# Performance work log

Measured on AMD Instinct MI355X. Metric: run time of the kernel, lower is better.

Reference implementation:

```python
import jax, jax.numpy as jnp
import numpy as np

N_NODES = 10000
N_EDGES = 160000
F_IN = 50          # PPI num_features
H = 4              # attention heads
C_BODY = 256       # body GAT out channels per head -> concat 1024
C_HEAD = 64        # head GAT out channels per head -> concat 256
T = 121            # PPI num_classes (one task head each)
D_BODY = H * C_BODY   # 1024
D_HEAD = H * C_HEAD   # 256


def setup_inputs() -> dict:
    key = jax.random.key(0)
    ks = jax.random.split(key, 18)
    inv = lambda f: 1.0 / np.sqrt(f)
    x = jax.random.normal(ks[0], (N_NODES, F_IN), dtype=jnp.float32)
    edge_index = jax.random.randint(ks[1], (2, N_EDGES), 0, N_NODES, dtype=jnp.int64)
    # body GATConv(50 -> 256, heads=4)
    W_body = jax.random.normal(ks[2], (F_IN, H, C_BODY), jnp.float32) * inv(F_IN)
    a_src_body = jax.random.normal(ks[3], (H, C_BODY), jnp.float32) * 0.1
    a_dst_body = jax.random.normal(ks[4], (H, C_BODY), jnp.float32) * 0.1
    b_body = jnp.zeros((D_BODY,), jnp.float32)
    # body Linear(50 -> 1024)
    Wfc_body = jax.random.normal(ks[5], (F_IN, D_BODY), jnp.float32) * inv(F_IN)
    bfc_body = jnp.zeros((D_BODY,), jnp.float32)
    # stacked per-task head GATConv(1024 -> 64, heads=4)
    Wh = jax.random.normal(ks[6], (T, D_BODY, H, C_HEAD), jnp.float32) * inv(D_BODY)
    a_src_h = jax.random.normal(ks[7], (T, H, C_HEAD), jnp.float32) * 0.1
    a_dst_h = jax.random.normal(ks[8], (T, H, C_HEAD), jnp.float32) * 0.1
    b_h = jnp.zeros((T, D_HEAD), jnp.float32)
    # stacked per-task Linear(1024 -> 256)
    W1 = jax.random.normal(ks[9], (T, D_BODY, D_HEAD), jnp.float32) * inv(D_BODY)
    b1 = jnp.zeros((T, D_HEAD), jnp.float32)
    # stacked per-task Linear(256 -> 2)
    W2 = jax.random.normal(ks[10], (T, D_HEAD, 2), jnp.float32) * inv(D_HEAD)
    b2 = jnp.zeros((T, 2), jnp.float32)
    return dict(x=x, edge_index=edge_index,
                W_body=W_body, a_src_body=a_src_body, a_dst_body=a_dst_body, b_body=b_body,
                Wfc_body=Wfc_body, bfc_body=bfc_body,
                Wh=Wh, a_src_h=a_src_h, a_dst_h=a_dst_h, b_h=b_h,
                W1=W1, b1=b1, W2=W2, b2=b2)


def gat_conv(x, W, a_src, a_dst, bias, src, dst, num_nodes):
    """PyG GATConv (concat=True, negative_slope=0.2). src/dst include self loops."""
    h = jnp.einsum('nf,fhc->nhc', x, W)                      # [N,H,C]
    al_src = jnp.sum(h * a_src, axis=-1)                     # [N,H]
    al_dst = jnp.sum(h * a_dst, axis=-1)                     # [N,H]
    e = jax.nn.leaky_relu(al_src[src] + al_dst[dst], 0.2)    # [E,H]
    # segment softmax over incoming edges of each target node
    m = jax.lax.stop_gradient(jax.ops.segment_max(e, dst, num_segments=num_nodes))
    ex = jnp.exp(e - m[dst])
    denom = jax.ops.segment_sum(ex, dst, num_segments=num_nodes)
    alpha = ex / (denom[dst] + 1e-16)                        # [E,H]
    out = jax.ops.segment_sum(alpha[:, :, None] * h[src], dst, num_segments=num_nodes)
    return out.reshape(num_nodes, -1) + bias                 # [N,H*C]


def reference(x, edge_index, W_body, a_src_body, a_dst_body, b_body,
              Wfc_body, bfc_body, Wh, a_src_h, a_dst_h, b_h, W1, b1, W2, b2):
    n = x.shape[0]
    loops = jnp.arange(n, dtype=edge_index.dtype)
    src = jnp.concatenate([edge_index[0], loops])   # add_self_loops=True
    dst = jnp.concatenate([edge_index[1], loops])
    x1 = jax.nn.elu(gat_conv(x, W_body, a_src_body, a_dst_body, b_body, src, dst, n)
                    + x @ Wfc_body + bfc_body)      # [N,1024]

    def head(params):
        Wh_t, as_t, ad_t, bh_t, W1_t, b1_t, W2_t, b2_t = params
        xh = jax.nn.elu(gat_conv(x1, Wh_t, as_t, ad_t, bh_t, src, dst, n)
                        + x1 @ W1_t + b1_t)         # [N,256]
        return xh @ W2_t + b2_t                     # [N,2]

    out = jax.lax.map(head, (Wh, a_src_h, a_dst_h, b_h, W1, b1, W2, b2))
    return out  # [T, N, 2], stacked version of the original list of 121 outputs
```

## Files before the change

kernel.cpp:

```cpp
#include <hip/hip_runtime.h>

typedef unsigned short u16;
typedef unsigned int u32;
typedef __attribute__((ext_vector_type(8))) short short8;
typedef __attribute__((ext_vector_type(4))) float f32x4;

#define NN 10000
#define NE 160000
#define ET 170000
#define FI 50
#define DB 1024
#define NT 121

static __device__ __forceinline__ float bf2f(u16 b) { return __uint_as_float(((u32)b) << 16); }
static __device__ __forceinline__ u16 f2bf(float f) {
  u32 u = __float_as_uint(f);
  u += 0x7FFFu + ((u >> 16) & 1u);
  return (u16)(u >> 16);
}
static __device__ __forceinline__ float eluf(float x) { return x > 0.f ? x : __expf(x) - 1.f; }
static __device__ __forceinline__ float lrelu(float x) { return x > 0.f ? x : 0.2f * x; }

__device__ __forceinline__ void gload16(const void* g, void* l) {
  __builtin_amdgcn_global_load_lds((const __attribute__((address_space(1))) u32*)g,
                                   (__attribute__((address_space(3))) u32*)l, 16, 0, 0);
}

__global__ __launch_bounds__(256) void k_detect(const int* __restrict__ ei, int* flag) {
  int any = 0;
  for (int i = threadIdx.x; i < NE; i += 256) any |= ei[2 * i + 1];
  if (any) flag[0] = 1;
}

__global__ __launch_bounds__(256) void k_deg(const int* __restrict__ ei, const int* __restrict__ flag,
                                             int* deg) {
  int e = blockIdx.x * 256 + threadIdx.x;
  if (e >= ET) return;
  int is32 = flag[0];
  int d = (e < NE) ? (is32 ? ei[NE + e] : ei[2 * (NE + e)]) : (e - NE);
  atomicAdd(&deg[d], 1);
}

__global__ __launch_bounds__(256) void k_scan(const int* __restrict__ deg, int* __restrict__ rowptr) {
  __shared__ int ps[256];
  int tid = threadIdx.x;
  int s = 0;
  for (int i = 0; i < 40; i++) { int idx = tid * 40 + i; if (idx < NN) s += deg[idx]; }
  ps[tid] = s;
  __syncthreads();
  if (tid == 0) {
    int run = 0;
    for (int i = 0; i < 256; i++) { int v = ps[i]; ps[i] = run; run += v; }
    rowptr[NN] = run;
  }
  __syncthreads();
  int run = ps[tid];
  for (int i = 0; i < 40; i++) {
    int idx = tid * 40 + i;
    if (idx < NN) { rowptr[idx] = run; run += deg[idx]; }
  }
}

__global__ __launch_bounds__(256) void k_fill(const int* __restrict__ ei, const int* __restrict__ flag,
                                              const int* __restrict__ rowptr, int* fill, int* csr) {
  int e = blockIdx.x * 256 + threadIdx.x;
  if (e >= ET) return;
  int is32 = flag[0];
  int s, d;
  if (e < NE) { s = is32 ? ei[e] : ei[2 * e]; d = is32 ? ei[NE + e] : ei[2 * (NE + e)]; }
  else { s = d = e - NE; }
  int pos = atomicAdd(&fill[d], 1);
  csr[rowptr[d] + pos] = s;
}

__global__ __launch_bounds__(256) void k_body_gemm(const float* __restrict__ x, const float* __restrict__ Wb,
                                                   const float* __restrict__ Wfc,
                                                   u16* __restrict__ h_body, u16* __restrict__ xfc) {
  __shared__ float xs[32][52];
  int tid = threadIdx.x;
  int m0 = blockIdx.x * 32;
  for (int i = tid; i < 32 * FI; i += 256) {
    int r = i / FI, c = i - r * FI;
    int row = m0 + r; if (row > NN - 1) row = NN - 1;
    xs[r][c] = x[(size_t)row * FI + c];
  }
  __syncthreads();
  int col = blockIdx.y * 256 + tid;
  const float* Wp; u16* op;
  if (col < DB) { Wp = Wb + col; op = h_body + col; }
  else { Wp = Wfc + (col - DB); op = xfc + (col - DB); }
  float acc[32];
  #pragma unroll
  for (int m = 0; m < 32; m++) acc[m] = 0.f;
  for (int k = 0; k < FI; k++) {
    float wv = Wp[(size_t)k * DB];
    #pragma unroll
    for (int m = 0; m < 32; m++) acc[m] += xs[m][k] * wv;
  }
  #pragma unroll
  for (int m = 0; m < 32; m++) {
    int row = m0 + m;
    if (row < NN) op[(size_t)row * DB] = f2bf(acc[m]);
  }
}

__global__ __launch_bounds__(64) void k_body_al(const u16* __restrict__ h_body, const float* __restrict__ as,
                                                const float* __restrict__ ad, float* __restrict__ al) {
  int n = blockIdx.x, l = threadIdx.x;
  const u16* hr = h_body + (size_t)n * DB + l * 16;
  const float* ap = as + l * 16;
  const float* dp = ad + l * 16;
  float ss = 0.f, sd = 0.f;
  #pragma unroll
  for (int i = 0; i < 16; i++) { float hv = bf2f(hr[i]); ss += hv * ap[i]; sd += hv * dp[i]; }
  #pragma unroll
  for (int o = 1; o < 16; o <<= 1) { ss += __shfl_xor(ss, o); sd += __shfl_xor(sd, o); }
  if ((l & 15) == 0) { int h = l >> 4; al[(size_t)n * 8 + h] = ss; al[(size_t)n * 8 + 4 + h] = sd; }
}

__global__ __launch_bounds__(256) void k_body_agg(const u16* __restrict__ h_body, const u16* __restrict__ xfc,
                                                  const float* __restrict__ al, const int* __restrict__ rowptr,
                                                  const int* __restrict__ csr, const float* __restrict__ bb,
                                                  const float* __restrict__ bfc, u16* __restrict__ x1b) {
  __shared__ float wl[256];
  __shared__ int sl[64];
  int n = blockIdx.x, tid = threadIdx.x;
  int c0 = tid * 4, h = tid >> 6;
  float acc0 = 0, acc1 = 0, acc2 = 0, acc3 = 0, wsum = 0;
  int beg = rowptr[n], end = rowptr[n + 1];
  for (int base = beg; base < end; base += 64) {
    int cnt = end - base; if (cnt > 64) cnt = 64;
    int slot = tid >> 2, hh = tid & 3;
    if (slot < cnt) {
      int s = csr[base + slot];
      if (hh == 0) sl[slot] = s;
      float e = al[(size_t)s * 8 + hh] + al[(size_t)n * 8 + 4 + hh];
      wl[slot * 4 + hh] = __expf(lrelu(e));
    }
    __syncthreads();
    for (int j = 0; j < cnt; j++) {
      float wv = wl[j * 4 + h];
      int s = sl[j];
      ushort4 hv = *(const ushort4*)(h_body + (size_t)s * DB + c0);
      acc0 += wv * bf2f(hv.x); acc1 += wv * bf2f(hv.y);
      acc2 += wv * bf2f(hv.z); acc3 += wv * bf2f(hv.w);
      wsum += wv;
    }
    __syncthreads();
  }
  float inv = 1.f / (wsum + 1e-16f);
  ushort4 xf = *(const ushort4*)(xfc + (size_t)n * DB + c0);
  ushort4 o;
  o.x = f2bf(eluf(acc0 * inv + bb[c0 + 0] + bf2f(xf.x) + bfc[c0 + 0]));
  o.y = f2bf(eluf(acc1 * inv + bb[c0 + 1] + bf2f(xf.y) + bfc[c0 + 1]));
  o.z = f2bf(eluf(acc2 * inv + bb[c0 + 2] + bf2f(xf.z) + bfc[c0 + 2]));
  o.w = f2bf(eluf(acc3 * inv + bb[c0 + 3] + bf2f(xf.w) + bfc[c0 + 3]));
  *(ushort4*)(x1b + (size_t)n * DB + c0) = o;
}

__global__ __launch_bounds__(256) void k_trans_w(const float* __restrict__ Wh, const float* __restrict__ W1,
                                                 u16* __restrict__ Wt, int t0) {
  __shared__ float tile[64][65];
  int t = t0 + blockIdx.z;
  int k0 = blockIdx.x * 64, n0 = blockIdx.y * 64;
  const float* Wsrc = (n0 < 256) ? (Wh + (size_t)t * 1024 * 256 + n0)
                                 : (W1 + (size_t)t * 1024 * 256 + (n0 - 256));
  int tid = threadIdx.x;
  for (int i = tid; i < 4096; i += 256) {
    int kr = i >> 6, nc = i & 63;
    tile[kr][nc] = Wsrc[(size_t)(k0 + kr) * 256 + nc];
  }
  __syncthreads();
  u16* dst = Wt + ((size_t)blockIdx.z * 512 + n0) * 1024 + k0;
  for (int i = tid; i < 4096; i += 256) {
    int nr = i >> 6, kc = i & 63;
    dst[(size_t)nr * 1024 + kc] = f2bf(tile[kc][nr]);
  }
}

__global__ __launch_bounds__(512) void k_task_gemm(const u16* __restrict__ x1b, const u16* __restrict__ Wt,
                                                   u16* __restrict__ HT, int Gc) {
  __shared__ alignas(16) u16 As[4096];
  __shared__ alignas(16) u16 Bs[8192];
  int tid = threadIdx.x;
  int sRow = tid >> 2, sQ = tid & 3;
  int m0 = blockIdx.x * 128;
  int bn = blockIdx.y;
  int r0 = m0 + sRow; if (r0 > NN - 1) r0 = NN - 1;
  const u16* Ag = x1b + (size_t)r0 * 1024 + sQ * 8;
  const u16* BgBase = Wt + ((size_t)(bn * 256) + sRow) * 1024 + sQ * 8;
  u16* Al  = As + tid * 8;
  u16* Bl0 = Bs + tid * 8;
  u16* Bl1 = Bs + 4096 + tid * 8;
  int wv = tid >> 6, lane = tid & 63;
  int wm = wv >> 2, wn = wv & 3;
  const u16* Ar = As + ((wm * 64) + (lane & 15)) * 32 + (lane >> 4) * 8;
  const u16* Br = Bs + ((wn * 64) + (lane & 15)) * 32 + (lane >> 4) * 8;

  int zbeg = blockIdx.z * 2;
  int zend = zbeg + 2; if (zend > Gc) zend = Gc;
  for (int z = zbeg; z < zend; z++) {
    const u16* Bg0 = BgBase + (size_t)z * 524288;
    const u16* Bg1 = Bg0 + 131072;
    f32x4 acc[4][4];
    #pragma unroll
    for (int a = 0; a < 4; a++)
      #pragma unroll
      for (int b = 0; b < 4; b++) acc[a][b] = (f32x4){0.f, 0.f, 0.f, 0.f};
    for (int k0 = 0; k0 < 1024; k0 += 32) {
      gload16(Ag + k0, Al);
      gload16(Bg0 + k0, Bl0);
      gload16(Bg1 + k0, Bl1);
      __syncthreads();
      short8 af[4], bfr[4];
      #pragma unroll
      for (int a = 0; a < 4; a++) af[a] = *(const short8*)(Ar + a * 512);
      #pragma unroll
      for (int a = 0; a < 4; a++) bfr[a] = *(const short8*)(Br + a * 512);
      #pragma unroll
      for (int a = 0; a < 4; a++)
        #pragma unroll
        for (int b = 0; b < 4; b++)
          acc[a][b] = __builtin_amdgcn_mfma_f32_16x16x32_bf16(af[a], bfr[b], acc[a][b], 0, 0, 0);
      __syncthreads();
    }
    u16* Hb = HT + (size_t)z * NN * 512;
    #pragma unroll
    for (int a = 0; a < 4; a++) {
      int rbase = m0 + wm * 64 + a * 16 + (lane >> 4) * 4;
      #pragma unroll
      for (int b = 0; b < 4; b++) {
        int col = bn * 256 + wn * 64 + b * 16 + (lane & 15);
        #pragma unroll
        for (int r = 0; r < 4; r++) {
          int row = rbase + r;
          if (row < NN) Hb[(size_t)row * 512 + col] = f2bf(acc[a][b][r]);
        }
      }
    }
  }
}

__global__ __launch_bounds__(64) void k_task_al(const u16* __restrict__ HT, const float* __restrict__ ash,
                                                const float* __restrict__ adh, float* __restrict__ ALt, int t0) {
  int n = blockIdx.x, g = blockIdx.y, l = threadIdx.x;
  int t = t0 + g;
  const u16* row = HT + ((size_t)g * NN + n) * 512 + l * 4;
  ushort4 v = *(const ushort4*)row;
  int h = l >> 4, cl = (l * 4) & 63;
  const float* ap = ash + ((size_t)t * 4 + h) * 64 + cl;
  const float* dp = adh + ((size_t)t * 4 + h) * 64 + cl;
  float f0 = bf2f(v.x), f1 = bf2f(v.y), f2 = bf2f(v.z), f3 = bf2f(v.w);
  float ss = f0 * ap[0] + f1 * ap[1] + f2 * ap[2] + f3 * ap[3];
  float sd = f0 * dp[0] + f1 * dp[1] + f2 * dp[2] + f3 * dp[3];
  #pragma unroll
  for (int o = 1; o < 16; o <<= 1) { ss += __shfl_xor(ss, o); sd += __shfl_xor(sd, o); }
  if ((l & 15) == 0) {
    float* dst = ALt + ((size_t)g * NN + n) * 8;
    dst[h] = ss; dst[4 + h] = sd;
  }
}

__global__ __launch_bounds__(64) void k_task_agg_out(const u16* __restrict__ HT, const float* __restrict__ ALt,
                                                     const int* __restrict__ rowptr, const int* __restrict__ csr,
                                                     const float* __restrict__ bh, const float* __restrict__ b1,
                                                     const float* __restrict__ W2, const float* __restrict__ b2,
                                                     float* __restrict__ out, int t0) {
  __shared__ float wl[256];
  __shared__ int sl[64];
  int n = blockIdx.x, g = blockIdx.y, l = threadIdx.x;
  int t = t0 + g;
  int c0 = l * 4, h = l >> 4;
  const u16* Hb = HT + (size_t)g * NN * 512;
  const float* ALg = ALt + (size_t)g * NN * 8;
  float ad0 = ALg[(size_t)n * 8 + 4], ad1 = ALg[(size_t)n * 8 + 5];
  float ad2 = ALg[(size_t)n * 8 + 6], ad3 = ALg[(size_t)n * 8 + 7];
  float acc0 = 0, acc1 = 0, acc2 = 0, acc3 = 0, wsum = 0;
  int beg = rowptr[n], end = rowptr[n + 1];
  for (int base = beg; base < end; base += 64) {
    int cnt = end - base; if (cnt > 64) cnt = 64;
    if (l < cnt) {
      int s = csr[base + l];
      sl[l] = s;
      const float* alsp = ALg + (size_t)s * 8;
      wl[l * 4 + 0] = __expf(lrelu(alsp[0] + ad0));
      wl[l * 4 + 1] = __expf(lrelu(alsp[1] + ad1));
      wl[l * 4 + 2] = __expf(lrelu(alsp[2] + ad2));
      wl[l * 4 + 3] = __expf(lrelu(alsp[3] + ad3));
    }
    __syncthreads();
    for (int j = 0; j < cnt; j++) {
      float wv = wl[j * 4 + h];
      int s = sl[j];
      ushort4 hv = *(const ushort4*)(Hb + (size_t)s * 512 + c0);
      acc0 += wv * bf2f(hv.x); acc1 += wv * bf2f(hv.y);
      acc2 += wv * bf2f(hv.z); acc3 += wv * bf2f(hv.w);
      wsum += wv;
    }
    __syncthreads();
  }
  float inv = 1.f / (wsum + 1e-16f);
  ushort4 fc = *(const ushort4*)(Hb + (size_t)n * 512 + 256 + c0);
  const float* bhp = bh + (size_t)t * 256 + c0;
  const float* b1p = b1 + (size_t)t * 256 + c0;
  const float* w2p = W2 + ((size_t)t * 256 + c0) * 2;
  float o0 = 0, o1 = 0, xv;
  xv = eluf(acc0 * inv + bhp[0] + bf2f(fc.x) + b1p[0]); o0 += xv * w2p[0]; o1 += xv * w2p[1];
  xv = eluf(acc1 * inv + bhp[1] + bf2f(fc.y) + b1p[1]); o0 += xv * w2p[2]; o1 += xv * w2p[3];
  xv = eluf(acc2 * inv + bhp[2] + bf2f(fc.z) + b1p[2]); o0 += xv * w2p[4]; o1 += xv * w2p[5];
  xv = eluf(acc3 * inv + bhp[3] + bf2f(fc.w) + b1p[3]); o0 += xv * w2p[6]; o1 += xv * w2p[7];
  #pragma unroll
  for (int o = 1; o < 64; o <<= 1) { o0 += __shfl_xor(o0, o); o1 += __shfl_xor(o1, o); }
  if (l == 0) {
    float* op = out + ((size_t)t * NN + n) * 2;
    op[0] = o0 + b2[t * 2];
    op[1] = o1 + b2[t * 2 + 1];
  }
}

extern "C" void kernel_launch(void* const* d_in, const int* in_sizes, int n_in,
                              void* d_out, int out_size, void* d_ws, size_t ws_size,
                              hipStream_t stream) {
  const float* x   = (const float*)d_in[0];
  const int*   ei  = (const int*)  d_in[1];
  const float* Wb  = (const float*)d_in[2];
  const float* asb = (const float*)d_in[3];
  const float* adb = (const float*)d_in[4];
  const float* bb  = (const float*)d_in[5];
  const float* Wfc = (const float*)d_in[6];
  const float* bfc = (const float*)d_in[7];
  const float* Wh  = (const float*)d_in[8];
  const float* ash = (const float*)d_in[9];
  const float* adh = (const float*)d_in[10];
  const float* bh  = (const float*)d_in[11];
  const float* W1  = (const float*)d_in[12];
  const float* b1  = (const float*)d_in[13];
  const float* W2  = (const float*)d_in[14];
  const float* b2  = (const float*)d_in[15];
  float* out = (float*)d_out;

  char* w = (char*)d_ws;
  size_t off = 0;
  auto take = [&](size_t b) { size_t o = off; off = (off + b + 255) & ~(size_t)255; return o; };
  u16*   x1b    = (u16*)  (w + take((size_t)NN * DB * 2));
  float* albody = (float*)(w + take((size_t)NN * 8 * 4));
  int*   flag   = (int*)  (w + take(4 + NN * 4 + NN * 4));
  int*   deg    = flag + 1;
  int*   fill   = deg + NN;
  int*   rowptr = (int*)  (w + take((NN + 1) * 4));
  int*   csr    = (int*)  (w + take((size_t)ET * 4));
  size_t Rbase = off;
  u16* h_body = (u16*)(w + Rbase);
  u16* xfc    = h_body + (size_t)NN * DB;
  const size_t perTask = 1048576 + 10240000 + 320000;
  size_t avail = ws_size > Rbase ? ws_size - Rbase : 0;
  int G = (int)(avail / perTask);
  if (G < 1) G = 1;
  if (G > NT) G = NT;
  u16*   Wt  = (u16*)(w + Rbase);
  u16*   HT  = Wt + (size_t)G * 524288;
  float* ALt = (float*)(HT + (size_t)G * 5120000);

  hipMemsetAsync(flag, 0, 4 + NN * 4 + NN * 4, stream);
  k_detect<<<1, 256, 0, stream>>>(ei, flag);
  k_deg<<<(ET + 255) / 256, 256, 0, stream>>>(ei, flag, deg);
  k_scan<<<1, 256, 0, stream>>>(deg, rowptr);
  k_fill<<<(ET + 255) / 256, 256, 0, stream>>>(ei, flag, rowptr, fill, csr);
  k_body_gemm<<<dim3(313, 8), 256, 0, stream>>>(x, Wb, Wfc, h_body, xfc);
  k_body_al<<<NN, 64, 0, stream>>>(h_body, asb, adb, albody);
  k_body_agg<<<NN, 256, 0, stream>>>(h_body, xfc, albody, rowptr, csr, bb, bfc, x1b);

  for (int t0 = 0; t0 < NT; t0 += G) {
    int Gc = NT - t0; if (Gc > G) Gc = G;
    k_trans_w<<<dim3(16, 8, Gc), 256, 0, stream>>>(Wh, W1, Wt, t0);
    k_task_gemm<<<dim3(79, 2, (Gc + 1) / 2), 512, 0, stream>>>(x1b, Wt, HT, Gc);
    k_task_al<<<dim3(NN, Gc), 64, 0, stream>>>(HT, ash, adh, ALt, t0);
    k_task_agg_out<<<dim3(NN, Gc), 64, 0, stream>>>(HT, ALt, rowptr, csr, bh, b1, W2, b2, out, t0);
  }
}
```

Before: 3.967 ms.

## Pipeline task GEMM with 4-stage LDS ring, 256-row tiles, swizzle and XCD remap

Rewrites the per-task GEMM to use 256x256 output tiles per workgroup with a 4-slot LDS ring buffer, prefetching three K-steps ahead and waiting on vmcnt instead of doing a full load-sync each step. LDS is written and read with an XOR-style quad swizzle to avoid bank conflicts, MFMA sections get raised priority, and a flat grid is remapped so neighbouring tiles land on the same XCD. The aim is to hide global-to-LDS latency and improve reuse and L2 locality. In exchange each workgroup uses much more LDS and more accumulator registers, which lowers occupancy.

After: 3.531 ms. 11.0% less time.

```diff
diff --git a/kernel.cpp b/kernel.cpp
--- a/kernel.cpp
+++ b/kernel.cpp
@@ -178,56 +178,100 @@
   }
 }
 
-__global__ __launch_bounds__(512) void k_task_gemm(const u16* __restrict__ x1b, const u16* __restrict__ Wt,
-                                                   u16* __restrict__ HT, int Gc) {
-  __shared__ alignas(16) u16 As[4096];
-  __shared__ alignas(16) u16 Bs[8192];
+__global__ __launch_bounds__(512, 2) void k_task_gemm(const u16* __restrict__ x1b, const u16* __restrict__ Wt,
+                                                      u16* __restrict__ HT, int Gc, int zp) {
+  __shared__ alignas(16) u16 AsF[4 * 8192];
+  __shared__ alignas(16) u16 BsF[4 * 8192];
   int tid = threadIdx.x;
+  int wgid = blockIdx.x;
+  int cpx = 10 * zp;
+  int j = (wgid & 7) * cpx + (wgid >> 3);
+  int tpm = 2 * zp;
+  int bm = j / tpm, idx = j - bm * tpm;
+  int bn = idx & 1, bz = idx >> 1;
+  int m0 = bm * 256;
   int sRow = tid >> 2, sQ = tid & 3;
-  int m0 = blockIdx.x * 128;
-  int bn = blockIdx.y;
-  int r0 = m0 + sRow; if (r0 > NN - 1) r0 = NN - 1;
-  const u16* Ag = x1b + (size_t)r0 * 1024 + sQ * 8;
-  const u16* BgBase = Wt + ((size_t)(bn * 256) + sRow) * 1024 + sQ * 8;
-  u16* Al  = As + tid * 8;
-  u16* Bl0 = Bs + tid * 8;
-  u16* Bl1 = Bs + 4096 + tid * 8;
+  int sA = (sQ + (sRow >> 1)) & 3;
+  int dstOff = sRow * 32 + sQ * 8;
+  int ra0 = m0 + sRow;       if (ra0 > NN - 1) ra0 = NN - 1;
+  int ra1 = m0 + 128 + sRow; if (ra1 > NN - 1) ra1 = NN - 1;
+  const u16* Ag0 = x1b + (size_t)ra0 * 1024 + sA * 8;
+  const u16* Ag1 = x1b + (size_t)ra1 * 1024 + sA * 8;
+  const u16* BgB0 = Wt + ((size_t)(bn * 256 + sRow)) * 1024 + sA * 8;
+  const u16* BgB1 = Wt + ((size_t)(bn * 256 + 128 + sRow)) * 1024 + sA * 8;
   int wv = tid >> 6, lane = tid & 63;
   int wm = wv >> 2, wn = wv & 3;
-  const u16* Ar = As + ((wm * 64) + (lane & 15)) * 32 + (lane >> 4) * 8;
-  const u16* Br = Bs + ((wn * 64) + (lane & 15)) * 32 + (lane >> 4) * 8;
-
-  int zbeg = blockIdx.z * 2;
+  int qRead = ((lane >> 4) - ((lane & 15) >> 1)) & 3;
+  int AfragOff = (wm * 128 + (lane & 15)) * 32 + qRead * 8;
+  int BfragOff = (wn * 64 + (lane & 15)) * 32 + qRead * 8;
+
+  int zbeg = bz * 2;
   int zend = zbeg + 2; if (zend > Gc) zend = Gc;
   for (int z = zbeg; z < zend; z++) {
-    const u16* Bg0 = BgBase + (size_t)z * 524288;
-    const u16* Bg1 = Bg0 + 131072;
-    f32x4 acc[4][4];
+    const u16* Bg0 = BgB0 + (size_t)z * 524288;
+    const u16* Bg1 = BgB1 + (size_t)z * 524288;
+    f32x4 acc[8][4];
     #pragma unroll
-    for (int a = 0; a < 4; a++)
+    for (int a = 0; a < 8; a++)
       #pragma unroll
       for (int b = 0; b < 4; b++) acc[a][b] = (f32x4){0.f, 0.f, 0.f, 0.f};
-    for (int k0 = 0; k0 < 1024; k0 += 32) {
-      gload16(Ag + k0, Al);
-      gload16(Bg0 + k0, Bl0);
-      gload16(Bg1 + k0, Bl1);
-      __syncthreads();
+
+#define STAGE(kt_, slot_)                                    \
+    do {                                                     \
+      int _k = (kt_) * 32;                                   \
+      u16* _as = AsF + (slot_) * 8192 + dstOff;              \
+      u16* _bs = BsF + (slot_) * 8192 + dstOff;              \
+      gload16(Ag0 + _k, _as);                                \
+      gload16(Ag1 + _k, _as + 4096);                         \
+      gload16(Bg0 + _k, _bs);                                \
+      gload16(Bg1 + _k, _bs + 4096);                         \
+    } while (0)
+
+    STAGE(0, 0);
+    STAGE(1, 1);
+    STAGE(2, 2);
+
+    for (int kt = 0; kt < 32; kt++) {
+      if (kt < 30)       asm volatile("s_waitcnt vmcnt(8)" ::: "memory");
+      else if (kt == 30) asm volatile("s_waitcnt vmcnt(4)" ::: "memory");
+      else               asm volatile("s_waitcnt vmcnt(0)" ::: "memory");
+      __builtin_amdgcn_s_barrier();
+      __builtin_amdgcn_sched_barrier(0);
+      int s = kt & 3;
+      const u16* Ac = AsF + s * 8192 + AfragOff;
+      const u16* Bc = BsF + s * 8192 + BfragOff;
+      if (kt + 3 < 32) STAGE(kt + 3, (kt + 3) & 3);
       short8 af[4], bfr[4];
       #pragma unroll
-      for (int a = 0; a < 4; a++) af[a] = *(const short8*)(Ar + a * 512);
-      #pragma unroll
-      for (int a = 0; a < 4; a++) bfr[a] = *(const short8*)(Br + a * 512);
+      for (int a = 0; a < 4; a++) af[a] = *(const short8*)(Ac + a * 512);
+      #pragma unroll
+      for (int b = 0; b < 4; b++) bfr[b] = *(const short8*)(Bc + b * 512);
+      __builtin_amdgcn_s_setprio(1);
       #pragma unroll
       for (int a = 0; a < 4; a++)
         #pragma unroll
         for (int b = 0; b < 4; b++)
           acc[a][b] = __builtin_amdgcn_mfma_f32_16x16x32_bf16(af[a], bfr[b], acc[a][b], 0, 0, 0);
-      __syncthreads();
-    }
+      __builtin_amdgcn_s_setprio(0);
+      __builtin_amdgcn_sched_barrier(0);
+      __builtin_amdgcn_s_barrier();
+      __builtin_amdgcn_sched_barrier(0);
+      #pragma unroll
+      for (int a = 0; a < 4; a++) af[a] = *(const short8*)(Ac + (4 + a) * 512);
+      __builtin_amdgcn_s_setprio(1);
+      #pragma unroll
+      for (int a = 0; a < 4; a++)
+        #pragma unroll
+        for (int b = 0; b < 4; b++)
+          acc[4 + a][b] = __builtin_amdgcn_mfma_f32_16x16x32_bf16(af[a], bfr[b], acc[4 + a][b], 0, 0, 0);
+      __builtin_amdgcn_s_setprio(0);
+      __builtin_amdgcn_sched_barrier(0);
+    }
+#undef STAGE
     u16* Hb = HT + (size_t)z * NN * 512;
     #pragma unroll
-    for (int a = 0; a < 4; a++) {
-      int rbase = m0 + wm * 64 + a * 16 + (lane >> 4) * 4;
+    for (int a = 0; a < 8; a++) {
+      int rbase = m0 + wm * 128 + a * 16 + (lane >> 4) * 4;
       #pragma unroll
       for (int b = 0; b < 4; b++) {
         int col = bn * 256 + wn * 64 + b * 16 + (lane & 15);
@@ -372,8 +416,9 @@
 
   for (int t0 = 0; t0 < NT; t0 += G) {
     int Gc = NT - t0; if (Gc > G) Gc = G;
+    int zp = (Gc + 1) / 2;
     k_trans_w<<<dim3(16, 8, Gc), 256, 0, stream>>>(Wh, W1, Wt, t0);
-    k_task_gemm<<<dim3(79, 2, (Gc + 1) / 2), 512, 0, stream>>>(x1b, Wt, HT, Gc);
+    k_task_gemm<<<80 * zp, 512, 0, stream>>>(x1b, Wt, HT, Gc, zp);
     k_task_al<<<dim3(NN, Gc), 64, 0, stream>>>(HT, ash, adh, ALt, t0);
     k_task_agg_out<<<dim3(NN, Gc), 64, 0, stream>>>(HT, ALt, rowptr, csr, bh, b1, W2, b2, out, t0);
   }
```

## Triple-buffer task GEMM LDS loads with swizzled layout and single barrier

Applied to the files above, without the earlier changes.

The per-task GEMM now uses a three-slot LDS ring filled by async global-to-LDS loads issued two k-steps ahead. Each step waits with vmcnt and a single barrier instead of two __syncthreads. The LDS layout is XOR-style swizzled on both the store and fragment-read sides to cut bank conflicts. MFMA issue priority is raised and launch bounds request 4 waves per SIMD, at the cost of three times the LDS footprint, which may limit how many blocks fit per CU.

After: 3.868 ms. 2.5% less time.

```diff
diff --git a/kernel.cpp b/kernel.cpp
--- a/kernel.cpp
+++ b/kernel.cpp
@@ -178,24 +178,25 @@
   }
 }
 
-__global__ __launch_bounds__(512) void k_task_gemm(const u16* __restrict__ x1b, const u16* __restrict__ Wt,
-                                                   u16* __restrict__ HT, int Gc) {
-  __shared__ alignas(16) u16 As[4096];
-  __shared__ alignas(16) u16 Bs[8192];
+__global__ __launch_bounds__(512, 4) void k_task_gemm(const u16* __restrict__ x1b, const u16* __restrict__ Wt,
+                                                      u16* __restrict__ HT, int Gc) {
+  __shared__ alignas(16) u16 As[3][4096];
+  __shared__ alignas(16) u16 Bs[3][8192];
   int tid = threadIdx.x;
   int sRow = tid >> 2, sQ = tid & 3;
+  int sA = (sQ + (sRow >> 1)) & 3;
   int m0 = blockIdx.x * 128;
   int bn = blockIdx.y;
   int r0 = m0 + sRow; if (r0 > NN - 1) r0 = NN - 1;
-  const u16* Ag = x1b + (size_t)r0 * 1024 + sQ * 8;
-  const u16* BgBase = Wt + ((size_t)(bn * 256) + sRow) * 1024 + sQ * 8;
-  u16* Al  = As + tid * 8;
-  u16* Bl0 = Bs + tid * 8;
-  u16* Bl1 = Bs + 4096 + tid * 8;
+  const u16* Ag = x1b + (size_t)r0 * 1024 + sA * 8;
+  const u16* BgBase = Wt + ((size_t)(bn * 256) + sRow) * 1024 + sA * 8;
+  int dstOff = tid * 8;
   int wv = tid >> 6, lane = tid & 63;
   int wm = wv >> 2, wn = wv & 3;
-  const u16* Ar = As + ((wm * 64) + (lane & 15)) * 32 + (lane >> 4) * 8;
-  const u16* Br = Bs + ((wn * 64) + (lane & 15)) * 32 + (lane >> 4) * 8;
+  int q = ((lane >> 4) - ((lane & 15) >> 1)) & 3;
+  int fragOff = (lane & 15) * 32 + q * 8;
+  int AfO = (wm * 64) * 32 + fragOff;
+  int BfO = (wn * 64) * 32 + fragOff;
 
   int zbeg = blockIdx.z * 2;
   int zend = zbeg + 2; if (zend > Gc) zend = Gc;
@@ -207,23 +208,42 @@
     for (int a = 0; a < 4; a++)
       #pragma unroll
       for (int b = 0; b < 4; b++) acc[a][b] = (f32x4){0.f, 0.f, 0.f, 0.f};
-    for (int k0 = 0; k0 < 1024; k0 += 32) {
-      gload16(Ag + k0, Al);
-      gload16(Bg0 + k0, Bl0);
-      gload16(Bg1 + k0, Bl1);
-      __syncthreads();
+
+#define STAGE(kt_, slot_)                              \
+    do {                                               \
+      int _k = (kt_) * 32;                             \
+      gload16(Ag + _k, &As[slot_][dstOff]);            \
+      gload16(Bg0 + _k, &Bs[slot_][dstOff]);           \
+      gload16(Bg1 + _k, &Bs[slot_][4096 + dstOff]);    \
+    } while (0)
+
+    STAGE(0, 0);
+    STAGE(1, 1);
+
+    #pragma unroll
+    for (int kt = 0; kt < 32; kt++) {
+      if (kt < 31) asm volatile("s_waitcnt vmcnt(3)" ::: "memory");
+      else         asm volatile("s_waitcnt vmcnt(0)" ::: "memory");
+      __builtin_amdgcn_s_barrier();
+      __builtin_amdgcn_sched_barrier(0);
+      int s = kt % 3;
+      if (kt + 2 < 32) STAGE(kt + 2, (kt + 2) % 3);
+      const u16* Ac = &As[s][0] + AfO;
+      const u16* Bc = &Bs[s][0] + BfO;
       short8 af[4], bfr[4];
       #pragma unroll
-      for (int a = 0; a < 4; a++) af[a] = *(const short8*)(Ar + a * 512);
+      for (int a = 0; a < 4; a++) af[a] = *(const short8*)(Ac + a * 512);
       #pragma unroll
-      for (int a = 0; a < 4; a++) bfr[a] = *(const short8*)(Br + a * 512);
+      for (int b = 0; b < 4; b++) bfr[b] = *(const short8*)(Bc + b * 512);
+      __builtin_amdgcn_s_setprio(1);
       #pragma unroll
       for (int a = 0; a < 4; a++)
         #pragma unroll
         for (int b = 0; b < 4; b++)
           acc[a][b] = __builtin_amdgcn_mfma_f32_16x16x32_bf16(af[a], bfr[b], acc[a][b], 0, 0, 0);
-      __syncthreads();
-    }
+      __builtin_amdgcn_s_setprio(0);
+    }
+#undef STAGE
     u16* Hb = HT + (size_t)z * NN * 512;
     #pragma unroll
     for (int a = 0; a < 4; a++) {
@@ -238,6 +258,7 @@
         }
       }
     }
+    __syncthreads();
   }
 }
 
```
